# Optimization experiments

Measured on AMD Instinct MI355X. Metric: run time of the kernel, lower is better.

## Reference

```python
import jax, jax.numpy as jnp
import numpy as np

N_NODES = 50000


def _gcn_conv(x, W, b, src, dst, n):
    """PyG GCNConv: add self-loops, symmetric normalization, sum-aggregate."""
    h = x @ W  # [N, out_dim] dense transform first (out_dim <= in_dim path)
    loop = jnp.arange(n, dtype=src.dtype)
    src_sl = jnp.concatenate([src, loop])
    dst_sl = jnp.concatenate([dst, loop])
    # degree computed on destination nodes (incl. self-loops)
    deg = jax.ops.segment_sum(jnp.ones_like(dst_sl, dtype=h.dtype), dst_sl, num_segments=n)
    dinv = jnp.where(deg > 0, jax.lax.rsqrt(deg), 0.0)
    norm = dinv[src_sl] * dinv[dst_sl]  # [E+N]
    msgs = h[src_sl] * norm[:, None]  # gather + scale, [E+N, out_dim]
    out = jax.ops.segment_sum(msgs, dst_sl, num_segments=n)  # scatter-add
    return out + b


def setup_inputs() -> dict:
    key = jax.random.key(0)
    k0, k1, k2, k3 = jax.random.split(key, 4)
    d = 256
    E = 400000
    scale = 1.0 / np.sqrt(d)
    x = jax.random.normal(k0, (N_NODES, d), dtype=jnp.float32)
    edge_index = jax.random.randint(k1, (2, E), 0, N_NODES, dtype=jnp.int64)
    W1 = jax.random.normal(k2, (d, d), dtype=jnp.float32) * scale
    b1 = jnp.zeros((d,), dtype=jnp.float32)
    W2 = jax.random.normal(k3, (d, d), dtype=jnp.float32) * scale
    b2 = jnp.zeros((d,), dtype=jnp.float32)
    return {"x": x, "edge_index": edge_index, "W1": W1, "b1": b1, "W2": W2, "b2": b2}


def reference(x, edge_index, W1, b1, W2, b2):
    src, dst = edge_index[0], edge_index[1]
    h = _gcn_conv(x, W1, b1, src, dst, N_NODES)
    h = jax.nn.relu(h)
    h = _gcn_conv(h, W2, b2, src, dst, N_NODES)
    h = jax.nn.relu(h)
    return h
```

## Files before the change

kernel.cpp:

```cpp
#include <hip/hip_runtime.h>
#include <stdint.h>

typedef __bf16 bf16_t;
typedef bf16_t bf16x4 __attribute__((ext_vector_type(4)));
typedef bf16_t bf16x8 __attribute__((ext_vector_type(8)));
typedef float f32x4 __attribute__((ext_vector_type(4)));

#define DIM 256
#define NNODES 50000

__device__ __forceinline__ int detect_f64(const int* __restrict__ ei) {
    int v = ei[2 * (threadIdx.x & 63) + 1];
    unsigned long long m = __ballot(v == 0);
    return __popcll(m) > 32;
}

__device__ __forceinline__ int load_edge(const int* __restrict__ ei, int E, int f64,
                                         int which , int e) {
    int v = f64 ? ei[(size_t)which * 2 * E + 2 * (size_t)e]
                : ei[(size_t)which * E + (size_t)e];
    return min(max(v, 0), NNODES - 1);
}


__global__ __launch_bounds__(256) void prep_kernel(int* __restrict__ counts,
                                                   const float* __restrict__ W1,
                                                   const float* __restrict__ W2,
                                                   bf16_t* __restrict__ Wf1,
                                                   bf16_t* __restrict__ Wf2, int n) {
    const int nb = (NNODES + 255) / 256;
    int b = blockIdx.x, t = threadIdx.x;
    if (b < nb) {
        int idx = b * 256 + t;
        if (idx < n) counts[idx] = 0;
    } else {
        int cw = b - nb;
        const float* W = (cw & 256) ? W2 : W1;
        bf16_t* Wf = (cw & 256) ? Wf2 : Wf1;
        int k = cw & 255;
        int s = k >> 5, quad = (k >> 3) & 3, j = k & 7;
        int nt = t >> 4, m = t & 15;
        Wf[s * 8192 + (nt * 64 + quad * 16 + m) * 8 + j] = (bf16_t)W[k * DIM + t];
    }
}


__global__ __launch_bounds__(256, 4) void gemm1_hist_kernel(const float* __restrict__ X,
                                                            const bf16_t* __restrict__ Wf,
                                                            bf16_t* __restrict__ H, int tiles,
                                                            int gemm_blocks,
                                                            const int* __restrict__ ei, int E,
                                                            int* __restrict__ counts) {
    __shared__ bf16_t sB[8192];
    if ((int)blockIdx.x >= gemm_blocks) {
        int f64 = detect_f64(ei);
        int e = (blockIdx.x - gemm_blocks) * 256 + threadIdx.x;
        if (e < E) atomicAdd(&counts[load_edge(ei, E, f64, 1, e)], 1);
        return;
    }

    int tid = threadIdx.x;
    int wave = tid >> 6, lane = tid & 63;
    int m = lane & 15, quad = lane >> 4;
    int tile = blockIdx.x * 4 + wave;
    bool active = tile < tiles;
    int arow = (min(tile, tiles - 1)) * 16 + m;

    f32x4 acc[16] = {};

    for (int s = 0; s < 8; s++) {
        __syncthreads();
        {
            const bf16x8* g = (const bf16x8*)Wf + s * 1024;
            bf16x8* d = (bf16x8*)sB;
            #pragma unroll
            for (int it = 0; it < 4; it++) d[tid + it * 256] = g[tid + it * 256];
        }
        __syncthreads();

        bf16x8 a;
        const f32x4* xp = (const f32x4*)(X + (size_t)arow * DIM + s * 32 + quad * 8);
        f32x4 x0 = xp[0], x1 = xp[1];
        #pragma unroll
        for (int j = 0; j < 4; j++) { a[j] = (bf16_t)x0[j]; a[j + 4] = (bf16_t)x1[j]; }

        #pragma unroll
        for (int nt = 0; nt < 16; nt++) {
            bf16x8 b = *(const bf16x8*)(sB + nt * 512 + lane * 8);
            acc[nt] = __builtin_amdgcn_mfma_f32_16x16x32_bf16(a, b, acc[nt], 0, 0, 0);
        }
    }

    if (active) {
        int rowb = tile * 16 + quad * 4;
        #pragma unroll
        for (int nt = 0; nt < 16; nt++) {
            #pragma unroll
            for (int r = 0; r < 4; r++) {
                H[(size_t)(rowb + r) * DIM + nt * 16 + m] = (bf16_t)acc[nt][r];
            }
        }
    }
}


__global__ __launch_bounds__(256) void scan_kernel(const int* __restrict__ counts,
                                                   int* __restrict__ offsets,
                                                   int* __restrict__ cursor,
                                                   float* __restrict__ dinv, int n) {
    __shared__ int red[256];
    __shared__ int sm[256];
    int b = blockIdx.x, t = threadIdx.x;

    int part = 0;
    const int4* c4 = (const int4*)counts;
    int lim = b * 64;
    for (int j = t; j < lim; j += 256) {
        int4 v = c4[j];
        part += v.x + v.y + v.z + v.w;
    }
    red[t] = part;
    __syncthreads();
    #pragma unroll
    for (int off = 128; off > 0; off >>= 1) {
        if (t < off) red[t] += red[t + off];
        __syncthreads();
    }
    int base = red[0];

    int idx = b * 256 + t;
    int v = (idx < n) ? counts[idx] : 0;
    sm[t] = v;
    __syncthreads();
    #pragma unroll
    for (int off = 1; off < 256; off <<= 1) {
        int u = (t >= off) ? sm[t - off] : 0;
        __syncthreads();
        sm[t] += u;
        __syncthreads();
    }
    if (idx < n) {
        int incl = base + sm[t];
        offsets[idx + 1] = incl;
        cursor[idx] = incl - v;
        dinv[idx] = rsqrtf((float)(v + 1));
    }
    if (idx == 0) offsets[0] = 0;
}

__global__ void scatter_kernel(const int* __restrict__ ei, int E,
                               const float* __restrict__ dinv, int* __restrict__ cursor,
                               int2* __restrict__ csr_e) {
    int f64 = detect_f64(ei);
    int e = blockIdx.x * blockDim.x + threadIdx.x;
    if (e < E) {
        int s = load_edge(ei, E, f64, 0, e);
        int d = load_edge(ei, E, f64, 1, e);
        int pos = atomicAdd(&cursor[d], 1);
        if (pos >= 0 && pos < E) {
            int2 v;
            v.x = s;
            v.y = __float_as_int(dinv[s] * dinv[d]);
            csr_e[pos] = v;
        }
    }
}


__global__ __launch_bounds__(256, 4) void gemm_kernel(const bf16_t* __restrict__ Xv,
                                                      const bf16_t* __restrict__ Wf,
                                                      bf16_t* __restrict__ H, int tiles) {
    __shared__ bf16_t sB[8192];
    int tid = threadIdx.x;
    int wave = tid >> 6, lane = tid & 63;
    int m = lane & 15, quad = lane >> 4;
    int tile = blockIdx.x * 4 + wave;
    bool active = tile < tiles;
    int arow = (min(tile, tiles - 1)) * 16 + m;

    f32x4 acc[16] = {};

    for (int s = 0; s < 8; s++) {
        __syncthreads();
        {
            const bf16x8* g = (const bf16x8*)Wf + s * 1024;
            bf16x8* d = (bf16x8*)sB;
            #pragma unroll
            for (int it = 0; it < 4; it++) d[tid + it * 256] = g[tid + it * 256];
        }
        __syncthreads();

        bf16x8 a = *(const bf16x8*)(Xv + (size_t)arow * DIM + s * 32 + quad * 8);

        #pragma unroll
        for (int nt = 0; nt < 16; nt++) {
            bf16x8 b = *(const bf16x8*)(sB + nt * 512 + lane * 8);
            acc[nt] = __builtin_amdgcn_mfma_f32_16x16x32_bf16(a, b, acc[nt], 0, 0, 0);
        }
    }

    if (active) {
        int rowb = tile * 16 + quad * 4;
        #pragma unroll
        for (int nt = 0; nt < 16; nt++) {
            #pragma unroll
            for (int r = 0; r < 4; r++) {
                H[(size_t)(rowb + r) * DIM + nt * 16 + m] = (bf16_t)acc[nt][r];
            }
        }
    }
}


template <int OUT_BF16>
__global__ __launch_bounds__(256) void aggregate_kernel(const bf16_t* __restrict__ H,
                                                        const int* __restrict__ offsets,
                                                        const int2* __restrict__ csr_e,
                                                        const float* __restrict__ dinv,
                                                        const float* __restrict__ bias,
                                                        void* __restrict__ outv, int n) {
    int wg = threadIdx.x >> 5;
    int l = threadIdx.x & 31;
    int i = blockIdx.x * 8 + wg;
    if (i >= n) return;

    const char* Hb = (const char*)H;
    int doff = l * 16;

    auto cvt = [](bf16x4 v) -> f32x4 {
        f32x4 r;
        #pragma unroll
        for (int j = 0; j < 4; j++) r[j] = (float)v[j];
        return r;
    };
    auto lo4 = [](bf16x8 v) -> bf16x4 { return __builtin_shufflevector(v, v, 0, 1, 2, 3); };
    auto hi4 = [](bf16x8 v) -> bf16x4 { return __builtin_shufflevector(v, v, 4, 5, 6, 7); };

    float dii = dinv[i];
    bf16x8 selfv = *(const bf16x8*)(Hb + ((size_t)i << 9) + doff);
    f32x4 acc0 = cvt(lo4(selfv)) * (dii * dii);
    f32x4 acc1 = cvt(hi4(selfv)) * (dii * dii);

    int e0 = offsets[i], e1 = offsets[i + 1];
    int e = e0;
    for (; e + 8 <= e1; e += 8) {
        unsigned s[8]; float w[8];
        #pragma unroll
        for (int j = 0; j < 8; j++) {
            int2 t = csr_e[e + j];
            s[j] = min((unsigned)t.x, (unsigned)(NNODES - 1));
            w[j] = __int_as_float(t.y);
        }
        bf16x8 h[8];
        #pragma unroll
        for (int j = 0; j < 8; j++) {
            h[j] = *(const bf16x8*)(Hb + ((size_t)s[j] << 9) + doff);
        }
        __builtin_amdgcn_sched_barrier(0);
        #pragma unroll
        for (int j = 0; j < 8; j++) {
            acc0 += cvt(lo4(h[j])) * w[j];
            acc1 += cvt(hi4(h[j])) * w[j];
        }
    }
    if (e < e1) {
        unsigned s[8]; float w[8];
        #pragma unroll
        for (int j = 0; j < 8; j++) {
            bool valid = (e + j) < e1;
            int2 t = csr_e[valid ? e + j : e];
            if (!valid) { t.x = i; t.y = 0; }
            s[j] = min((unsigned)t.x, (unsigned)(NNODES - 1));
            w[j] = __int_as_float(t.y);
        }
        bf16x8 h[8];
        #pragma unroll
        for (int j = 0; j < 8; j++) {
            h[j] = *(const bf16x8*)(Hb + ((size_t)s[j] << 9) + doff);
        }
        __builtin_amdgcn_sched_barrier(0);
        #pragma unroll
        for (int j = 0; j < 8; j++) {
            acc0 += cvt(lo4(h[j])) * w[j];
            acc1 += cvt(hi4(h[j])) * w[j];
        }
    }

    const f32x4* bp = (const f32x4*)(bias + l * 8);
    acc0 += bp[0];
    acc1 += bp[1];
    #pragma unroll
    for (int j = 0; j < 4; j++) {
        acc0[j] = fmaxf(acc0[j], 0.0f);
        acc1[j] = fmaxf(acc1[j], 0.0f);
    }

    if (OUT_BF16) {
        bf16x8 o;
        #pragma unroll
        for (int j = 0; j < 4; j++) { o[j] = (bf16_t)acc0[j]; o[j + 4] = (bf16_t)acc1[j]; }
        *(bf16x8*)((bf16_t*)outv + (size_t)i * DIM + l * 8) = o;
    } else {
        float* op = (float*)outv + (size_t)i * DIM + l * 8;
        *(f32x4*)op = acc0;
        *(f32x4*)(op + 4) = acc1;
    }
}


extern "C" void kernel_launch(void* const* d_in, const int* in_sizes, int n_in,
                              void* d_out, int out_size, void* d_ws, size_t ws_size,
                              hipStream_t stream) {
    const float* x  = (const float*)d_in[0];
    const int*   ei = (const int*)d_in[1];
    const float* W1 = (const float*)d_in[2];
    const float* b1 = (const float*)d_in[3];
    const float* W2 = (const float*)d_in[4];
    const float* b2 = (const float*)d_in[5];
    float* out = (float*)d_out;

    const int n = NNODES;
    const int E = in_sizes[1] / 2;
    const int nb = (n + 255) / 256;

    char* ws = (char*)d_ws;
    size_t off = 0;
    auto alloc = [&](size_t bytes) -> char* {
        char* p = ws + off;
        off += (bytes + 255) & ~(size_t)255;
        return p;
    };
    float*  dinv     = (float*)alloc((size_t)n * 4);
    int*    counts   = (int*)alloc((size_t)n * 4);
    int*    offsets  = (int*)alloc((size_t)(n + 1) * 4);
    int*    cursor   = (int*)alloc((size_t)n * 4);
    int2*   csr_e    = (int2*)alloc((size_t)E * 8);
    bf16_t* Wf1      = (bf16_t*)alloc((size_t)DIM * DIM * 2);
    bf16_t* Wf2      = (bf16_t*)alloc((size_t)DIM * DIM * 2);
    bf16_t* P        = (bf16_t*)alloc((size_t)n * DIM * 2);
    bf16_t* X2       = (bf16_t*)alloc((size_t)n * DIM * 2);

    int tiles = (n + 15) / 16;
    int gemm_blocks = (tiles + 3) / 4;
    int hist_blocks = (E + 255) / 256;
    int agg_blocks = (n + 7) / 8;

    prep_kernel<<<nb + 512, 256, 0, stream>>>(counts, W1, W2, Wf1, Wf2, n);
    gemm1_hist_kernel<<<gemm_blocks + hist_blocks, 256, 0, stream>>>(x, Wf1, P, tiles,
                                                                     gemm_blocks, ei, E, counts);
    scan_kernel<<<nb, 256, 0, stream>>>(counts, offsets, cursor, dinv, n);
    scatter_kernel<<<hist_blocks, 256, 0, stream>>>(ei, E, dinv, cursor, csr_e);
    aggregate_kernel<1><<<agg_blocks, 256, 0, stream>>>(P, offsets, csr_e, dinv, b1, X2, n);
    gemm_kernel<<<gemm_blocks, 256, 0, stream>>>(X2, Wf2, P, tiles);
    aggregate_kernel<0><<<agg_blocks, 256, 0, stream>>>(P, offsets, csr_e, dinv, b2, out, n);
}
```

Baseline: 252.0 us.

## Pair GEMM tiles per wave, fuse scatter into GEMM1, skip padded gathers

Each wave now computes two 16-row tiles, so every LDS B fragment read feeds two MFMAs. Launch bounds drop to 3 blocks per SM to make room for the doubled accumulators. The histogram becomes its own kernel and the CSR scatter pass is fused into the first GEMM launch instead, so scatter atomics overlap the GEMM work. In the aggregate tail, padded lanes skip their H gather and use a zero weight instead of loading a dummy row.

```diff
diff --git a/kernel.cpp b/kernel.cpp
--- a/kernel.cpp
+++ b/kernel.cpp
@@ -21,7 +21,6 @@
                 : ei[(size_t)which * E + (size_t)e];
     return min(max(v, 0), NNODES - 1);
 }
-
 
 __global__ __launch_bounds__(256) void prep_kernel(int* __restrict__ counts,
                                                    const float* __restrict__ W1,
@@ -44,65 +43,11 @@
     }
 }
 
-
-__global__ __launch_bounds__(256, 4) void gemm1_hist_kernel(const float* __restrict__ X,
-                                                            const bf16_t* __restrict__ Wf,
-                                                            bf16_t* __restrict__ H, int tiles,
-                                                            int gemm_blocks,
-                                                            const int* __restrict__ ei, int E,
-                                                            int* __restrict__ counts) {
-    __shared__ bf16_t sB[8192];
-    if ((int)blockIdx.x >= gemm_blocks) {
-        int f64 = detect_f64(ei);
-        int e = (blockIdx.x - gemm_blocks) * 256 + threadIdx.x;
-        if (e < E) atomicAdd(&counts[load_edge(ei, E, f64, 1, e)], 1);
-        return;
-    }
-
-    int tid = threadIdx.x;
-    int wave = tid >> 6, lane = tid & 63;
-    int m = lane & 15, quad = lane >> 4;
-    int tile = blockIdx.x * 4 + wave;
-    bool active = tile < tiles;
-    int arow = (min(tile, tiles - 1)) * 16 + m;
-
-    f32x4 acc[16] = {};
-
-    for (int s = 0; s < 8; s++) {
-        __syncthreads();
-        {
-            const bf16x8* g = (const bf16x8*)Wf + s * 1024;
-            bf16x8* d = (bf16x8*)sB;
-            #pragma unroll
-            for (int it = 0; it < 4; it++) d[tid + it * 256] = g[tid + it * 256];
-        }
-        __syncthreads();
-
-        bf16x8 a;
-        const f32x4* xp = (const f32x4*)(X + (size_t)arow * DIM + s * 32 + quad * 8);
-        f32x4 x0 = xp[0], x1 = xp[1];
-        #pragma unroll
-        for (int j = 0; j < 4; j++) { a[j] = (bf16_t)x0[j]; a[j + 4] = (bf16_t)x1[j]; }
-
-        #pragma unroll
-        for (int nt = 0; nt < 16; nt++) {
-            bf16x8 b = *(const bf16x8*)(sB + nt * 512 + lane * 8);
-            acc[nt] = __builtin_amdgcn_mfma_f32_16x16x32_bf16(a, b, acc[nt], 0, 0, 0);
-        }
-    }
-
-    if (active) {
-        int rowb = tile * 16 + quad * 4;
-        #pragma unroll
-        for (int nt = 0; nt < 16; nt++) {
-            #pragma unroll
-            for (int r = 0; r < 4; r++) {
-                H[(size_t)(rowb + r) * DIM + nt * 16 + m] = (bf16_t)acc[nt][r];
-            }
-        }
-    }
-}
-
+__global__ void hist_kernel(const int* __restrict__ ei, int E, int* __restrict__ counts) {
+    int f64 = detect_f64(ei);
+    int e = blockIdx.x * blockDim.x + threadIdx.x;
+    if (e < E) atomicAdd(&counts[load_edge(ei, E, f64, 1, e)], 1);
+}
 
 __global__ __launch_bounds__(256) void scan_kernel(const int* __restrict__ counts,
                                                    int* __restrict__ offsets,
@@ -148,37 +93,21 @@
     if (idx == 0) offsets[0] = 0;
 }
 
-__global__ void scatter_kernel(const int* __restrict__ ei, int E,
-                               const float* __restrict__ dinv, int* __restrict__ cursor,
-                               int2* __restrict__ csr_e) {
-    int f64 = detect_f64(ei);
-    int e = blockIdx.x * blockDim.x + threadIdx.x;
-    if (e < E) {
-        int s = load_edge(ei, E, f64, 0, e);
-        int d = load_edge(ei, E, f64, 1, e);
-        int pos = atomicAdd(&cursor[d], 1);
-        if (pos >= 0 && pos < E) {
-            int2 v;
-            v.x = s;
-            v.y = __float_as_int(dinv[s] * dinv[d]);
-            csr_e[pos] = v;
-        }
-    }
-}
-
-
-__global__ __launch_bounds__(256, 4) void gemm_kernel(const bf16_t* __restrict__ Xv,
-                                                      const bf16_t* __restrict__ Wf,
-                                                      bf16_t* __restrict__ H, int tiles) {
-    __shared__ bf16_t sB[8192];
+template <bool F32A>
+__device__ __forceinline__ void gemm_body(const void* __restrict__ Xv,
+                                          const bf16_t* __restrict__ Wf,
+                                          bf16_t* __restrict__ H, int tiles, int bid,
+                                          bf16_t* sB) {
     int tid = threadIdx.x;
     int wave = tid >> 6, lane = tid & 63;
     int m = lane & 15, quad = lane >> 4;
-    int tile = blockIdx.x * 4 + wave;
-    bool active = tile < tiles;
-    int arow = (min(tile, tiles - 1)) * 16 + m;
-
-    f32x4 acc[16] = {};
+    int t0 = (bid * 4 + wave) * 2;
+    int t1 = t0 + 1;
+    bool act0 = t0 < tiles, act1 = t1 < tiles;
+    int ar0 = min(t0, tiles - 1) * 16 + m;
+    int ar1 = min(t1, tiles - 1) * 16 + m;
+
+    f32x4 acc0[16] = {}, acc1[16] = {};
 
     for (int s = 0; s < 8; s++) {
         __syncthreads();
@@ -190,25 +119,84 @@
         }
         __syncthreads();
 
-        bf16x8 a = *(const bf16x8*)(Xv + (size_t)arow * DIM + s * 32 + quad * 8);
+        bf16x8 a0, a1;
+        if (F32A) {
+            const f32x4* xp0 = (const f32x4*)((const float*)Xv + (size_t)ar0 * DIM + s * 32 + quad * 8);
+            const f32x4* xp1 = (const f32x4*)((const float*)Xv + (size_t)ar1 * DIM + s * 32 + quad * 8);
+            f32x4 x0 = xp0[0], x1 = xp0[1], y0 = xp1[0], y1 = xp1[1];
+            #pragma unroll
+            for (int j = 0; j < 4; j++) {
+                a0[j] = (bf16_t)x0[j]; a0[j + 4] = (bf16_t)x1[j];
+                a1[j] = (bf16_t)y0[j]; a1[j + 4] = (bf16_t)y1[j];
+            }
+        } else {
+            a0 = *(const bf16x8*)((const bf16_t*)Xv + (size_t)ar0 * DIM + s * 32 + quad * 8);
+            a1 = *(const bf16x8*)((const bf16_t*)Xv + (size_t)ar1 * DIM + s * 32 + quad * 8);
+        }
 
         #pragma unroll
         for (int nt = 0; nt < 16; nt++) {
             bf16x8 b = *(const bf16x8*)(sB + nt * 512 + lane * 8);
-            acc[nt] = __builtin_amdgcn_mfma_f32_16x16x32_bf16(a, b, acc[nt], 0, 0, 0);
-        }
-    }
-
-    if (active) {
-        int rowb = tile * 16 + quad * 4;
+            acc0[nt] = __builtin_amdgcn_mfma_f32_16x16x32_bf16(a0, b, acc0[nt], 0, 0, 0);
+            acc1[nt] = __builtin_amdgcn_mfma_f32_16x16x32_bf16(a1, b, acc1[nt], 0, 0, 0);
+        }
+    }
+
+    if (act0) {
+        int rowb = t0 * 16 + quad * 4;
         #pragma unroll
         for (int nt = 0; nt < 16; nt++) {
             #pragma unroll
             for (int r = 0; r < 4; r++) {
-                H[(size_t)(rowb + r) * DIM + nt * 16 + m] = (bf16_t)acc[nt][r];
+                H[(size_t)(rowb + r) * DIM + nt * 16 + m] = (bf16_t)acc0[nt][r];
             }
         }
     }
+    if (act1) {
+        int rowb = t1 * 16 + quad * 4;
+        #pragma unroll
+        for (int nt = 0; nt < 16; nt++) {
+            #pragma unroll
+            for (int r = 0; r < 4; r++) {
+                H[(size_t)(rowb + r) * DIM + nt * 16 + m] = (bf16_t)acc1[nt][r];
+            }
+        }
+    }
+}
+
+__global__ __launch_bounds__(256, 3) void gemm1_scatter_kernel(const float* __restrict__ X,
+                                                               const bf16_t* __restrict__ Wf,
+                                                               bf16_t* __restrict__ H, int tiles,
+                                                               int gemm_blocks,
+                                                               const int* __restrict__ ei, int E,
+                                                               const float* __restrict__ dinv,
+                                                               int* __restrict__ cursor,
+                                                               int2* __restrict__ csr_e) {
+    __shared__ bf16_t sB[8192];
+    if ((int)blockIdx.x >= gemm_blocks) {
+        int f64 = detect_f64(ei);
+        int e = (blockIdx.x - gemm_blocks) * 256 + threadIdx.x;
+        if (e < E) {
+            int s = load_edge(ei, E, f64, 0, e);
+            int d = load_edge(ei, E, f64, 1, e);
+            int pos = atomicAdd(&cursor[d], 1);
+            if (pos >= 0 && pos < E) {
+                int2 v;
+                v.x = s;
+                v.y = __float_as_int(dinv[s] * dinv[d]);
+                csr_e[pos] = v;
+            }
+        }
+        return;
+    }
+    gemm_body<true>(X, Wf, H, tiles, blockIdx.x, sB);
+}
+
+__global__ __launch_bounds__(256, 3) void gemm2_kernel(const bf16_t* __restrict__ Xv,
+                                                       const bf16_t* __restrict__ Wf,
+                                                       bf16_t* __restrict__ H, int tiles) {
+    __shared__ bf16_t sB[8192];
+    gemm_body<false>(Xv, Wf, H, tiles, blockIdx.x, sB);
 }
 
 
@@ -264,19 +252,23 @@
         }
     }
     if (e < e1) {
-        unsigned s[8]; float w[8];
+        bf16x8 z;
+        #pragma unroll
+        for (int q = 0; q < 8; q++) z[q] = (bf16_t)0.0f;
+        unsigned s[8]; float w[8]; bool val[8];
         #pragma unroll
         for (int j = 0; j < 8; j++) {
             bool valid = (e + j) < e1;
+            val[j] = valid;
             int2 t = csr_e[valid ? e + j : e];
-            if (!valid) { t.x = i; t.y = 0; }
             s[j] = min((unsigned)t.x, (unsigned)(NNODES - 1));
-            w[j] = __int_as_float(t.y);
+            w[j] = valid ? __int_as_float(t.y) : 0.0f;
         }
         bf16x8 h[8];
         #pragma unroll
         for (int j = 0; j < 8; j++) {
-            h[j] = *(const bf16x8*)(Hb + ((size_t)s[j] << 9) + doff);
+            h[j] = z;
+            if (val[j]) h[j] = *(const bf16x8*)(Hb + ((size_t)s[j] << 9) + doff);
         }
         __builtin_amdgcn_sched_barrier(0);
         #pragma unroll
@@ -341,16 +333,17 @@
     bf16_t* X2       = (bf16_t*)alloc((size_t)n * DIM * 2);
 
     int tiles = (n + 15) / 16;
-    int gemm_blocks = (tiles + 3) / 4;
+    int pairs = (tiles + 1) / 2;
+    int gemm_blocks = (pairs + 3) / 4;
     int hist_blocks = (E + 255) / 256;
     int agg_blocks = (n + 7) / 8;
 
     prep_kernel<<<nb + 512, 256, 0, stream>>>(counts, W1, W2, Wf1, Wf2, n);
-    gemm1_hist_kernel<<<gemm_blocks + hist_blocks, 256, 0, stream>>>(x, Wf1, P, tiles,
-                                                                     gemm_blocks, ei, E, counts);
+    hist_kernel<<<hist_blocks, 256, 0, stream>>>(ei, E, counts);
     scan_kernel<<<nb, 256, 0, stream>>>(counts, offsets, cursor, dinv, n);
-    scatter_kernel<<<hist_blocks, 256, 0, stream>>>(ei, E, dinv, cursor, csr_e);
+    gemm1_scatter_kernel<<<gemm_blocks + hist_blocks, 256, 0, stream>>>(
+        x, Wf1, P, tiles, gemm_blocks, ei, E, dinv, cursor, csr_e);
     aggregate_kernel<1><<<agg_blocks, 256, 0, stream>>>(P, offsets, csr_e, dinv, b1, X2, n);
-    gemm_kernel<<<gemm_blocks, 256, 0, stream>>>(X2, Wf2, P, tiles);
+    gemm2_kernel<<<gemm_blocks, 256, 0, stream>>>(X2, Wf2, P, tiles);
     aggregate_kernel<0><<<agg_blocks, 256, 0, stream>>>(P, offsets, csr_e, dinv, b2, out, n);
 }
```

New measurement: 252.4 us. No clear change (+0.2%).
